# Performance work log

Measured on AMD Instinct MI355X. Metric: run time of the kernel, lower is better.

## Reference

```python
import jax, jax.numpy as jnp
import numpy as np

DATA_DIM = 128
UNITS = 512
LAYERS = 3
BATCH = 32
IN_STEPS = 1000   # int((T_input + 0.5*dt)//dt)
OUT_STEPS = 100   # int((T_output + 0.5*dt)//dt)


def setup_inputs() -> dict:
    key = jax.random.key(0)
    ks = jax.random.split(key, 16)
    d = {}
    d["x"] = jax.random.normal(ks[0], (BATCH, IN_STEPS, DATA_DIM), jnp.float32)
    in_dims = [DATA_DIM, UNITS, UNITS]
    i = 1
    for j in range(LAYERS):
        d[f"W{j}"] = jax.random.normal(ks[i], (in_dims[j], 3 * UNITS), jnp.float32) * 0.05; i += 1
        d[f"U{j}"] = jax.random.normal(ks[i], (UNITS, 3 * UNITS), jnp.float32) * 0.05; i += 1
        d[f"b{j}"] = jnp.zeros((2, 3 * UNITS), jnp.float32)
        d[f"s{j}"] = jax.random.normal(ks[i], (1, UNITS), jnp.float32); i += 1
    d["Wd"] = jax.random.normal(ks[i], (UNITS, DATA_DIM), jnp.float32) * 0.05
    d["bd"] = jnp.zeros((DATA_DIM,), jnp.float32)
    return d


def _gru_cell(x, h, W, U, b):
    # Keras GRUCell, reset_after=True (TF2 default)
    mx = x @ W + b[0]           # [B, 3U]
    mh = h @ U + b[1]           # [B, 3U]
    xz, xr, xh = jnp.split(mx, 3, axis=-1)
    hz, hr, hh = jnp.split(mh, 3, axis=-1)
    z = jax.nn.sigmoid(xz + hz)
    r = jax.nn.sigmoid(xr + hr)
    cand = jnp.tanh(xh + r * hh)
    return z * h + (1.0 - z) * cand


def reference(x, W0, U0, b0, s0, W1, U1, b1, s1, W2, U2, b2, s2, Wd, bd):
    params = [(W0, U0, b0), (W1, U1, b1), (W2, U2, b2)]
    B = x.shape[0]
    # learnable initial states, tiled over batch -> [L, B, U]
    h0 = jnp.stack([jnp.tile(s, (B, 1)) for s in (s0, s1, s2)])
    # model processes timesteps 0 .. in_steps-2 (last input step unused)
    xs = jnp.swapaxes(x[:, : IN_STEPS - 1, :], 0, 1)  # [T-1, B, D]

    def step(h, xt):
        hs = []
        inp = xt
        for j, (W, U, b) in enumerate(params):
            hj = _gru_cell(inp, h[j], W, U, b)
            hs.append(hj)
            inp = hj
        hn = jnp.stack(hs)  # [L, B, U]
        return hn, (inp, hn)

    _, (ys, hs) = jax.lax.scan(step, h0, xs)
    # outputs correspond to steps in_steps-out_steps-1 .. in_steps-2
    ys = ys[-OUT_STEPS:]   # [out_steps, B, U]
    hs = hs[-OUT_STEPS:]   # [out_steps, L, B, U]
    preds = ys @ Wd + bd   # [out_steps, B, D]
    predictions = jnp.swapaxes(preds, 0, 1)        # [B, out_steps, D]
    hidden = jnp.transpose(hs, (2, 0, 1, 3))       # [B, out_steps, L, U]
    return predictions, hidden
```

## Files before the change

### kernel.cpp

```cpp
#include <hip/hip_runtime.h>
#include <math.h>

#define B_   32
#define INS  1000
#define TS   999
#define D_   128
#define U_   512
#define G3   1536
#define OUTS 100
#define NB   208
#define NTHR 512

#define HBUF_OFF 0
#define HBUF_SZ  (4*3*512*32)
#define RING_OFF HBUF_SZ
#define RING_SZ  (4*1536*32)
#define BAR_OFF  (RING_OFF + RING_SZ)

#define PART_OFF  24576
#define STAGE_OFF 33792
#define SMEM_FLOATS 39936
#define PIDX4(s,g,c,e) ((((s)*4+(g))*8+(c))*36 + (e))
#define XBUF_OFF 12288

#define WT_STORE(p, v) __hip_atomic_store((p), (v), __ATOMIC_RELAXED, __HIP_MEMORY_SCOPE_AGENT)
#define CG_LOAD(p)     __hip_atomic_load((p), __ATOMIC_RELAXED, __HIP_MEMORY_SCOPE_AGENT)

#define GLOAD_LDS(G, L) __builtin_amdgcn_global_load_lds( \
  (const __attribute__((address_space(1))) void*)(G), \
  (__attribute__((address_space(3))) void*)(L), 16, 0, 0)

#define WAITV1 do { asm volatile("s_waitcnt vmcnt(1)" ::: "memory"); \
  __builtin_amdgcn_sched_barrier(0); } while (0)
#define WAITV0 do { asm volatile("s_waitcnt vmcnt(0)" ::: "memory"); \
  __builtin_amdgcn_sched_barrier(0); } while (0)

#define CHUNK_FMA(GH) { \
  const float* bp  = smem + STAGE_OFF + (c % 3) * 2048 + sub * 256 + eg * 4; \
  const float* wp2 = smem + (c * 64 + sub * 8) * 24 + c_l * 3; \
  _Pragma("unroll") \
  for (int rr = 0; rr < 8; ++rr) { \
    float4 av = *(const float4*)(bp + rr * 32); \
    float w0 = wp2[0], w1 = wp2[1], w2 = wp2[2]; \
    az[0]=fmaf(av.x,w0,az[0]); az[1]=fmaf(av.y,w0,az[1]); \
    az[2]=fmaf(av.z,w0,az[2]); az[3]=fmaf(av.w,w0,az[3]); \
    ar[0]=fmaf(av.x,w1,ar[0]); ar[1]=fmaf(av.y,w1,ar[1]); \
    ar[2]=fmaf(av.z,w1,ar[2]); ar[3]=fmaf(av.w,w1,ar[3]); \
    GH[0]=fmaf(av.x,w2,GH[0]); GH[1]=fmaf(av.y,w2,GH[1]); \
    GH[2]=fmaf(av.z,w2,GH[2]); GH[3]=fmaf(av.w,w2,GH[3]); \
    wp2 += 24; \
  } }

#define ISSUE_CHUNK(SRCBASE, CC) do { \
  const float* gsrc_ = (SRCBASE) + wv * 256 + lane * 4; \
  GLOAD_LDS(gsrc_, smem + STAGE_OFF + ((CC) % 3) * 2048 + wv * 256); \
} while (0)

__global__ void gru_init_kernel(const float* __restrict__ s0,
                                const float* __restrict__ s1,
                                const float* __restrict__ s2,
                                float* __restrict__ ws) {
  int g = blockIdx.x * 256 + threadIdx.x;
  if (g < 4096) { unsigned* bar = (unsigned*)(ws + BAR_OFF); bar[g] = 0u; }
  for (int i = g; i < 3 * 512 * 32; i += gridDim.x * 256) {
    int which = i / (512 * 32);
    int r = i - which * (512 * 32);
    int k = r >> 5, e = r & 31;
    const float* s = (which == 0) ? s0 : ((which == 1) ? s1 : s2);
    ws[HBUF_OFF + 3 * 49152 + which * 16384 + k * 32 + e] = s[k];
  }
}

__device__ __forceinline__ void wait_deps(unsigned* slots, int role, int t) {
  const int tid = threadIdx.x;
  const unsigned* p = nullptr; int tgt = 0;
  if (role < 0) {
    if (tid < 64)       { p = &slots[(0   + tid)       * 16]; tgt = t - 3; }
  } else if (role == 0) {
    if (tid < 64)       { p = &slots[(0   + tid)       * 16]; tgt = t;     }
    else if (tid < 80)  { p = &slots[(192 + tid - 64)  * 16]; tgt = t + 1; }
    else if (tid < 144) { p = &slots[(64  + tid - 80)  * 16]; tgt = t - 3; }
  } else if (role == 1) {
    if (tid < 64)       { p = &slots[(64  + tid)       * 16]; tgt = t;     }
    else if (tid < 128) { p = &slots[(0   + tid - 64)  * 16]; tgt = t + 1; }
    else if (tid < 192) { p = &slots[(128 + tid - 128) * 16]; tgt = t - 3; }
  } else {
    if (tid < 64)       { p = &slots[(128 + tid)       * 16]; tgt = t;     }
    else if (tid < 128) { p = &slots[(64  + tid - 64)  * 16]; tgt = t + 1; }
  }
  if (p && tgt > 0) {
    while ((int)CG_LOAD(p) < tgt) __builtin_amdgcn_s_sleep(1);
  }
  __syncthreads();
  if (role >= 0) {
    if (threadIdx.x == 0) __builtin_amdgcn_fence(__ATOMIC_ACQUIRE, "agent");
    __syncthreads();
  }
}

__device__ __forceinline__ void publish(unsigned* slots, int sidx, int t) {
  __syncthreads();
  if (threadIdx.x == 0) WT_STORE(&slots[sidx * 16], (unsigned)(t + 1));
}

__global__ __launch_bounds__(NTHR, 1) void gru_persist(
    const float* __restrict__ x,
    const float* __restrict__ W0c, const float* __restrict__ U0c, const float* __restrict__ b0c,
    const float* __restrict__ W1c, const float* __restrict__ U1c, const float* __restrict__ b1c,
    const float* __restrict__ W2c, const float* __restrict__ U2c, const float* __restrict__ b2c,
    const float* __restrict__ Wd, const float* __restrict__ bd,
    float* __restrict__ out, float* __restrict__ ws)
{
  float* hbuf = ws + HBUF_OFF;
  float* ring = ws + RING_OFF;
  unsigned* slots = (unsigned*)(ws + BAR_OFF);
  float* pred_out = out;
  float* hid_out  = out + B_ * OUTS * D_;

  const int bid = blockIdx.x;
  const int tid = threadIdx.x;

  int role, rb;
  if      (bid < 16)  { role = -1; rb = bid; }
  else if (bid < 80)  { role = 0;  rb = bid - 16; }
  else if (bid < 144) { role = 1;  rb = bid - 80; }
  else                { role = 2;  rb = bid - 144; }
  const int sidx = (role < 0) ? (192 + rb) : (role * 64 + rb);

  __shared__ float smem[SMEM_FLOATS];
  float* part = smem + PART_OFF;

  const int eg  = tid & 7;
  const int c_l = (tid >> 3) & 7;
  const int sub = tid >> 6;
  const int wv  = tid >> 6;
  const int lane = tid & 63;
  const int cb  = (rb & 7) * 8 + (rb >> 3);
  const int c0  = cb * 8;
  const int rc = tid >> 5;
  const int re = tid & 31;
  const int xb0 = ((rb & 7) * 2 + (rb >> 3)) * 96;
  const int cg3 = (tid & 31) * 3;
  const int e0  = (tid >> 5) * 2;

  const float *Wj = nullptr, *Ujp = nullptr, *bj = nullptr;
  if      (role == 0) { Ujp = U0c; bj = b0c; }
  else if (role == 1) { Wj = W1c; Ujp = U1c; bj = b1c; }
  else if (role == 2) { Wj = W2c; Ujp = U2c; bj = b2c; }

  if (role < 0) {
    for (int idx = tid; idx < 128 * 96; idx += NTHR)
      smem[idx] = W0c[(idx / 96) * G3 + xb0 + (idx % 96)];
    for (int f = tid; f < 1024; f += NTHR) {
      int e = f >> 5, d4 = (f & 31) * 4;
      *(float4*)(smem + XBUF_OFF + e * 128 + d4) =
          *(const float4*)(x + e * (INS * D_) + d4);
    }
  } else if (role == 0) {
    for (int idx = tid; idx < 512 * 24; idx += NTHR) {
      int row = idx / 24, cg = idx - row * 24, cc = cg / 3, g = cg - cc * 3;
      smem[idx] = Ujp[row * G3 + g * 512 + c0 + cc];
    }
  } else {
    for (int idx = tid; idx < 1024 * 24; idx += NTHR) {
      int row = idx / 24, cg = idx - row * 24, cc = cg / 3, g = cg - cc * 3;
      const float* mat = (row < 512) ? Wj : Ujp;
      int mr = (row < 512) ? row : row - 512;
      smem[idx] = mat[mr * G3 + g * 512 + c0 + cc];
    }
  }
  float bz = 0.f, br = 0.f, b0h = 0.f, b1h = 0.f;
  if (role >= 0 && tid < 256) {
    const int cg2 = c0 + rc;
    bz  = bj[cg2] + bj[G3 + cg2];
    br  = bj[512 + cg2] + bj[G3 + 512 + cg2];
    b0h = bj[1024 + cg2];
    b1h = bj[G3 + 1024 + cg2];
  }
  __syncthreads();

  for (int t = 0; t < TS; ++t) {
    wait_deps(slots, role, t);

    if (role < 0) {
      float4 xp0, xp1;
      const bool pf = (t + 1) < TS;
      if (pf) {
        int f0 = tid, f1 = tid + 512;
        xp0 = *(const float4*)(x + (f0 >> 5) * (INS * D_) + (t + 1) * D_ + (f0 & 31) * 4);
        xp1 = *(const float4*)(x + (f1 >> 5) * (INS * D_) + (t + 1) * D_ + (f1 & 31) * 4);
      }
      const float* xb = smem + XBUF_OFF + (t & 1) * 4096;
      float acc[3][2];
      #pragma unroll
      for (int c = 0; c < 3; ++c) { acc[c][0] = 0.f; acc[c][1] = 0.f; }
      #pragma unroll 4
      for (int k4 = 0; k4 < D_; k4 += 4) {
        float4 v0 = *(const float4*)(xb + e0 * 128 + k4);
        float4 v1 = *(const float4*)(xb + (e0 + 1) * 128 + k4);
        float xs0[4] = {v0.x, v0.y, v0.z, v0.w};
        float xs1[4] = {v1.x, v1.y, v1.z, v1.w};
        #pragma unroll
        for (int kk = 0; kk < 4; ++kk) {
          const float* wpx = smem + (k4 + kk) * 96 + cg3;
          float w0 = wpx[0], w1 = wpx[1], w2 = wpx[2];
          acc[0][0] = fmaf(xs0[kk], w0, acc[0][0]);
          acc[0][1] = fmaf(xs1[kk], w0, acc[0][1]);
          acc[1][0] = fmaf(xs0[kk], w1, acc[1][0]);
          acc[1][1] = fmaf(xs1[kk], w1, acc[1][1]);
          acc[2][0] = fmaf(xs0[kk], w2, acc[2][0]);
          acc[2][1] = fmaf(xs1[kk], w2, acc[2][1]);
        }
      }
      float* dst = ring + (t & 3) * (G3 * 32);
      #pragma unroll
      for (int c = 0; c < 3; ++c) {
        WT_STORE(dst + (xb0 + cg3 + c) * 32 + e0,     acc[c][0]);
        WT_STORE(dst + (xb0 + cg3 + c) * 32 + e0 + 1, acc[c][1]);
      }
      if (pf) {
        float* xw = smem + XBUF_OFF + ((t + 1) & 1) * 4096;
        int f0 = tid, f1 = tid + 512;
        *(float4*)(xw + (f0 >> 5) * 128 + (f0 & 31) * 4) = xp0;
        *(float4*)(xw + (f1 >> 5) * 128 + (f1 & 31) * 4) = xp1;
      }
    } else {
      const int j = role;
      const float* hownb = hbuf + ((t + 3) & 3) * 49152 + j * 16384;
      const float* hupb  = (j > 0) ? (hbuf + (t & 3) * 49152 + (j - 1) * 16384)
                                   : nullptr;

      float az[4] = {0,0,0,0}, ar[4] = {0,0,0,0};
      float axh[4] = {0,0,0,0}, ahh[4] = {0,0,0,0};

      if (j == 0) {
        ISSUE_CHUNK(hownb + 0 * 2048, 0);
        ISSUE_CHUNK(hownb + 1 * 2048, 1);
        #pragma unroll
        for (int c = 0; c < 8; ++c) {
          if (c < 7) WAITV1; else WAITV0;
          __builtin_amdgcn_s_barrier();
          __builtin_amdgcn_sched_barrier(0);
          if (c + 2 < 8) ISSUE_CHUNK(hownb + (c + 2) * 2048, c + 2);
          CHUNK_FMA(ahh);
        }
      } else {
        ISSUE_CHUNK(hupb + 0 * 2048, 0);
        ISSUE_CHUNK(hupb + 1 * 2048, 1);
        #pragma unroll
        for (int c = 0; c < 16; ++c) {
          if (c < 15) WAITV1; else WAITV0;
          __builtin_amdgcn_s_barrier();
          __builtin_amdgcn_sched_barrier(0);
          if (c + 2 < 16) {
            const float* nsrc = (c + 2 < 8) ? (hupb + (c + 2) * 2048)
                                            : (hownb + (c - 6) * 2048);
            ISSUE_CHUNK(nsrc, c + 2);
          }
          if (c < 8) { CHUNK_FMA(axh); } else { CHUNK_FMA(ahh); }
        }
      }

      float xz = 0.f, xr2 = 0.f, xhv0 = 0.f, hp = 0.f;
      if (tid < 256) {
        const int cg2 = c0 + rc;
        hp = hownb[cg2 * 32 + re];
        if (j == 0) {
          const float* r3 = ring + (t & 3) * (G3 * 32);
          xz   = r3[cg2 * 32 + re];
          xr2  = r3[(512 + cg2) * 32 + re];
          xhv0 = r3[(1024 + cg2) * 32 + re];
        }
      }

      *(float4*)&part[PIDX4(sub, 0, c_l, eg * 4)] = make_float4(az[0], az[1], az[2], az[3]);
      *(float4*)&part[PIDX4(sub, 1, c_l, eg * 4)] = make_float4(ar[0], ar[1], ar[2], ar[3]);
      if (j == 0) {
        *(float4*)&part[PIDX4(sub, 2, c_l, eg * 4)] = make_float4(ahh[0], ahh[1], ahh[2], ahh[3]);
      } else {
        *(float4*)&part[PIDX4(sub, 2, c_l, eg * 4)] = make_float4(axh[0], axh[1], axh[2], axh[3]);
        *(float4*)&part[PIDX4(sub, 3, c_l, eg * 4)] = make_float4(ahh[0], ahh[1], ahh[2], ahh[3]);
      }
      __syncthreads();

      if (tid < 256) {
        float gz = 0.f, gr = 0.f, xh = 0.f, hh = 0.f;
        #pragma unroll
        for (int s2 = 0; s2 < 8; ++s2) {
          gz += part[PIDX4(s2, 0, rc, re)];
          gr += part[PIDX4(s2, 1, rc, re)];
          if (j == 0) {
            hh += part[PIDX4(s2, 2, rc, re)];
          } else {
            xh += part[PIDX4(s2, 2, rc, re)];
            hh += part[PIDX4(s2, 3, rc, re)];
          }
        }
        const int cg2 = c0 + rc;
        const float xhv = (j == 0) ? xhv0 : xh;
        const float zi = gz + xz + bz;
        const float ri = gr + xr2 + br;
        const float z = 1.f / (1.f + expf(-zi));
        const float r = 1.f / (1.f + expf(-ri));
        const float cand = tanhf((xhv + b0h) + r * (hh + b1h));
        const float hn = z * hp + (1.f - z) * cand;
        WT_STORE(&hbuf[(t & 3) * 49152 + j * 16384 + cg2 * 32 + re], hn);
        if (t >= TS - OUTS) {
          WT_STORE(&hid_out[((re * OUTS + (t - (TS - OUTS))) * 3 + j) * U_ + cg2], hn);
        }
      }
    }
    publish(slots, sidx, t);
  }

  if (tid < 64) {
    while ((int)CG_LOAD(&slots[(128 + tid) * 16]) < TS) __builtin_amdgcn_s_sleep(1);
  }
  __syncthreads();
  if (tid == 0) __builtin_amdgcn_fence(__ATOMIC_ACQUIRE, "agent");
  __syncthreads();

  const int gt = bid * NTHR + tid;
  for (int o = gt; o < B_ * OUTS * D_; o += NB * NTHR) {
    int b  = o / (OUTS * D_);
    int r2 = o - b * (OUTS * D_);
    int s  = r2 >> 7;
    int dd = r2 & 127;
    const float* ys = hid_out + ((b * OUTS + s) * 3 + 2) * U_;
    float acc = bd[dd];
    #pragma unroll 4
    for (int k = 0; k < U_; k += 4) {
      float4 yv = *(const float4*)(ys + k);
      acc = fmaf(yv.x, Wd[(k    ) * D_ + dd], acc);
      acc = fmaf(yv.y, Wd[(k + 1) * D_ + dd], acc);
      acc = fmaf(yv.z, Wd[(k + 2) * D_ + dd], acc);
      acc = fmaf(yv.w, Wd[(k + 3) * D_ + dd], acc);
    }
    pred_out[o] = acc;
  }
}

extern "C" void kernel_launch(void* const* d_in, const int* in_sizes, int n_in,
                              void* d_out, int out_size, void* d_ws, size_t ws_size,
                              hipStream_t stream) {
  const float* x  = (const float*)d_in[0];
  const float* W0 = (const float*)d_in[1];
  const float* U0 = (const float*)d_in[2];
  const float* b0 = (const float*)d_in[3];
  const float* s0 = (const float*)d_in[4];
  const float* W1 = (const float*)d_in[5];
  const float* U1 = (const float*)d_in[6];
  const float* b1 = (const float*)d_in[7];
  const float* s1 = (const float*)d_in[8];
  const float* W2 = (const float*)d_in[9];
  const float* U2 = (const float*)d_in[10];
  const float* b2 = (const float*)d_in[11];
  const float* s2 = (const float*)d_in[12];
  const float* Wd = (const float*)d_in[13];
  const float* bd = (const float*)d_in[14];
  float* ws = (float*)d_ws;

  gru_init_kernel<<<192, 256, 0, stream>>>(s0, s1, s2, ws);
  gru_persist<<<NB, NTHR, 0, stream>>>(x, W0, U0, b0, W1, U1, b1,
                                       W2, U2, b2, Wd, bd, (float*)d_out, ws);
}
```

Baseline: 11.85 ms.

## Deepen LDS staging ring to six chunks and drop per-chunk block barriers

The recurrent h-chunk staging ring in LDS grows from 3 to 6 buffers, so six global-to-LDS loads are in flight before compute starts, and each wave waits only on its own vmcnt. Each wave loads and reads only its own slice of the staging buffer, so the per-chunk block-wide s_barrier is removed. The staging area is now aliased with the partial-sum buffer and placed directly after the weights for each role, with one __syncthreads added before the partial sums are written. The aim is to hide global-load latency and cut synchronisation on the latency-bound per-timestep path. The cost is more LDS use and reliance on waves being independent within the chunk loop.

Result: faster. 9.714 ms (-18.0%).

```diff
diff --git a/kernel.cpp b/kernel.cpp
--- a/kernel.cpp
+++ b/kernel.cpp
@@ -17,9 +17,7 @@
 #define RING_SZ  (4*1536*32)
 #define BAR_OFF  (RING_OFF + RING_SZ)
 
-#define PART_OFF  24576
-#define STAGE_OFF 33792
-#define SMEM_FLOATS 39936
+#define SMEM_FLOATS 36864
 #define PIDX4(s,g,c,e) ((((s)*4+(g))*8+(c))*36 + (e))
 #define XBUF_OFF 12288
 
@@ -30,14 +28,19 @@
   (const __attribute__((address_space(1))) void*)(G), \
   (__attribute__((address_space(3))) void*)(L), 16, 0, 0)
 
-#define WAITV1 do { asm volatile("s_waitcnt vmcnt(1)" ::: "memory"); \
+#define WAITVN(N) do { asm volatile("s_waitcnt vmcnt(" #N ")" ::: "memory"); \
   __builtin_amdgcn_sched_barrier(0); } while (0)
-#define WAITV0 do { asm volatile("s_waitcnt vmcnt(0)" ::: "memory"); \
-  __builtin_amdgcn_sched_barrier(0); } while (0)
-
-#define CHUNK_FMA(GH) { \
-  const float* bp  = smem + STAGE_OFF + (c % 3) * 2048 + sub * 256 + eg * 4; \
-  const float* wp2 = smem + (c * 64 + sub * 8) * 24 + c_l * 3; \
+#define WAIT_FOR(C, NCH) do { \
+  if ((NCH) - 1 - (C) >= 5)      { WAITVN(5); } \
+  else if ((NCH) - 1 - (C) == 4) { WAITVN(4); } \
+  else if ((NCH) - 1 - (C) == 3) { WAITVN(3); } \
+  else if ((NCH) - 1 - (C) == 2) { WAITVN(2); } \
+  else if ((NCH) - 1 - (C) == 1) { WAITVN(1); } \
+  else                           { WAITVN(0); } } while (0)
+
+#define CHUNK_FMA8(C, GH) { \
+  const float* bp  = stg + ((C) % 6) * 2048 + sub * 256 + eg * 4; \
+  const float* wp2 = smem + ((C) * 64 + sub * 8) * 24 + c_l * 3; \
   _Pragma("unroll") \
   for (int rr = 0; rr < 8; ++rr) { \
     float4 av = *(const float4*)(bp + rr * 32); \
@@ -53,7 +56,7 @@
 
 #define ISSUE_CHUNK(SRCBASE, CC) do { \
   const float* gsrc_ = (SRCBASE) + wv * 256 + lane * 4; \
-  GLOAD_LDS(gsrc_, smem + STAGE_OFF + ((CC) % 3) * 2048 + wv * 256); \
+  GLOAD_LDS(gsrc_, stg + ((CC) % 6) * 2048 + wv * 256); \
 } while (0)
 
 __global__ void gru_init_kernel(const float* __restrict__ s0,
@@ -128,7 +131,8 @@
   const int sidx = (role < 0) ? (192 + rb) : (role * 64 + rb);
 
   __shared__ float smem[SMEM_FLOATS];
-  float* part = smem + PART_OFF;
+  float* stg  = smem + ((role == 0) ? 12288 : 24576);
+  float* part = stg;
 
   const int eg  = tid & 7;
   const int c_l = (tid >> 3) & 7;
@@ -234,30 +238,31 @@
       float axh[4] = {0,0,0,0}, ahh[4] = {0,0,0,0};
 
       if (j == 0) {
-        ISSUE_CHUNK(hownb + 0 * 2048, 0);
-        ISSUE_CHUNK(hownb + 1 * 2048, 1);
+        ISSUE_CHUNK(hownb + 0 * 2048, 0); ISSUE_CHUNK(hownb + 1 * 2048, 1);
+        ISSUE_CHUNK(hownb + 2 * 2048, 2); ISSUE_CHUNK(hownb + 3 * 2048, 3);
+        ISSUE_CHUNK(hownb + 4 * 2048, 4); ISSUE_CHUNK(hownb + 5 * 2048, 5);
         #pragma unroll
         for (int c = 0; c < 8; ++c) {
-          if (c < 7) WAITV1; else WAITV0;
-          __builtin_amdgcn_s_barrier();
+          WAIT_FOR(c, 8);
+          CHUNK_FMA8(c, ahh);
           __builtin_amdgcn_sched_barrier(0);
-          if (c + 2 < 8) ISSUE_CHUNK(hownb + (c + 2) * 2048, c + 2);
-          CHUNK_FMA(ahh);
+          if (c + 6 < 8) ISSUE_CHUNK(hownb + (c + 6) * 2048, c + 6);
         }
       } else {
-        ISSUE_CHUNK(hupb + 0 * 2048, 0);
-        ISSUE_CHUNK(hupb + 1 * 2048, 1);
+        ISSUE_CHUNK(hupb + 0 * 2048, 0); ISSUE_CHUNK(hupb + 1 * 2048, 1);
+        ISSUE_CHUNK(hupb + 2 * 2048, 2); ISSUE_CHUNK(hupb + 3 * 2048, 3);
+        ISSUE_CHUNK(hupb + 4 * 2048, 4); ISSUE_CHUNK(hupb + 5 * 2048, 5);
         #pragma unroll
         for (int c = 0; c < 16; ++c) {
-          if (c < 15) WAITV1; else WAITV0;
-          __builtin_amdgcn_s_barrier();
+          WAIT_FOR(c, 16);
+          if (c < 8) { CHUNK_FMA8(c, axh); } else { CHUNK_FMA8(c, ahh); }
           __builtin_amdgcn_sched_barrier(0);
-          if (c + 2 < 16) {
-            const float* nsrc = (c + 2 < 8) ? (hupb + (c + 2) * 2048)
-                                            : (hownb + (c - 6) * 2048);
-            ISSUE_CHUNK(nsrc, c + 2);
+          if (c + 6 < 16) {
+            const int cc = c + 6;
+            const float* nsrc = (cc < 8) ? (hupb + cc * 2048)
+                                         : (hownb + (cc - 8) * 2048);
+            ISSUE_CHUNK(nsrc, cc);
           }
-          if (c < 8) { CHUNK_FMA(axh); } else { CHUNK_FMA(ahh); }
         }
       }
 
@@ -272,6 +277,8 @@
           xhv0 = r3[(1024 + cg2) * 32 + re];
         }
       }
+
+      __syncthreads();
 
       *(float4*)&part[PIDX4(sub, 0, c_l, eg * 4)] = make_float4(az[0], az[1], az[2], az[3]);
       *(float4*)&part[PIDX4(sub, 1, c_l, eg * 4)] = make_float4(ar[0], ar[1], ar[2], ar[3]);
```
